# Kernel tuning notes

Hardware: AMD Instinct MI355X
Metric: run time of the kernel (lower is better)

## Reference

```python
import jax, jax.numpy as jnp
import numpy as np
import math

D_MODEL = 2048
NUM_HEADS = 32
NUM_KV_HEADS = 8
D_K = D_MODEL // NUM_HEADS  # 64
GROUPS = NUM_HEADS // NUM_KV_HEADS  # 4
WINDOW = 512
ROPE_BASE = 10000.0


def setup_inputs() -> dict:
    key = jax.random.key(0)
    ks = jax.random.split(key, 5)
    B, T = 2, 2048
    x = jax.random.normal(ks[0], (B, T, D_MODEL), dtype=jnp.float32)
    s = 0.02  # typical init scale to keep logits sane
    Wq = jax.random.normal(ks[1], (D_MODEL, D_MODEL), dtype=jnp.float32) * s
    Wk = jax.random.normal(ks[2], (NUM_KV_HEADS * D_K, D_MODEL), dtype=jnp.float32) * s
    Wv = jax.random.normal(ks[3], (NUM_KV_HEADS * D_K, D_MODEL), dtype=jnp.float32) * s
    Wo = jax.random.normal(ks[4], (D_MODEL, D_MODEL), dtype=jnp.float32) * s
    return {"x": x, "Wq": Wq, "Wk": Wk, "Wv": Wv, "Wo": Wo}


def _rotate_half(t):
    half = t.shape[-1] // 2
    return jnp.concatenate([-t[..., half:], t[..., :half]], axis=-1)


def _rope_cos_sin(T, dtype):
    inv_freq = 1.0 / (ROPE_BASE ** (jnp.arange(0, D_K, 2, dtype=jnp.float32) / D_K))
    pos = jnp.arange(T, dtype=jnp.float32)
    freqs = pos[:, None] * inv_freq[None, :]            # [T, D_K/2]
    emb = jnp.concatenate([freqs, freqs], axis=-1)       # [T, D_K]
    return jnp.cos(emb).astype(dtype)[None, None], jnp.sin(emb).astype(dtype)[None, None]


def reference(x, Wq, Wk, Wv, Wo):
    B, T, D = x.shape
    # Projections (nn.Linear: x @ W.T)
    Q = (x @ Wq.T).reshape(B, T, NUM_HEADS, D_K).transpose(0, 2, 1, 3)     # [B,H,T,dk]
    K = (x @ Wk.T).reshape(B, T, NUM_KV_HEADS, D_K).transpose(0, 2, 1, 3)  # [B,KV,T,dk]
    V = (x @ Wv.T).reshape(B, T, NUM_KV_HEADS, D_K).transpose(0, 2, 1, 3)
    # RoPE
    cos, sin = _rope_cos_sin(T, x.dtype)
    Q = Q * cos + _rotate_half(Q) * sin
    K = K * cos + _rotate_half(K) * sin
    # GQA: fold group dim into Q instead of repeat_interleave on K/V (same math)
    Qg = Q.reshape(B, NUM_KV_HEADS, GROUPS, T, D_K)
    scale = math.sqrt(D_K)
    scores = jnp.einsum('bhgqd,bhkd->bhgqk', Qg, K) / scale  # [B,KV,G,T,T]
    # sliding-window causal mask: valid iff 0 <= q_pos - k_pos < WINDOW
    pos = jnp.arange(T)
    dist = pos[:, None] - pos[None, :]
    win_mask = (dist < 0) | (dist >= WINDOW)
    scores = jnp.where(win_mask[None, None, None], -jnp.inf, scores)
    attn = jax.nn.softmax(scores, axis=-1)
    out = jnp.einsum('bhgqk,bhkd->bhgqd', attn, V)
    out = out.reshape(B, NUM_HEADS, T, D_K).transpose(0, 2, 1, 3).reshape(B, T, D)
    return out @ Wo.T
```

## Files before the change

### kernel.cpp

```cpp
#include <hip/hip_runtime.h>
#include <hip/hip_bf16.h>
#include <cstdint>
#include <cstddef>

typedef __attribute__((ext_vector_type(4))) float f32x4;
typedef __attribute__((ext_vector_type(8))) short bf16x8;
typedef __attribute__((ext_vector_type(4))) int i32x4;
typedef void __attribute__((address_space(1)))* as1_void_p;
typedef void __attribute__((address_space(3)))* as3_void_p;

#define T_SEQ 2048
#define D_MODEL 2048
#define NUM_HEADS 32
#define NUM_KV 8
#define GROUPS 4
#define DK 64
#define WINDOW 512
#define BATCH 2

#define NEG_BIG (-30000.0f)

__device__ __forceinline__ unsigned short f2b(float f) {
    unsigned int u = __builtin_bit_cast(unsigned int, f);
    u = (u + 0x7FFFu + ((u >> 16) & 1u)) >> 16;
    return (unsigned short)u;
}

__device__ __forceinline__ unsigned int cvtpk_bf16(float lo, float hi) {
    unsigned int r;
    asm("v_cvt_pk_bf16_f32 %0, %1, %2" : "=v"(r) : "v"(lo), "v"(hi));
    return r;
}

__device__ __forceinline__ void load_lds16(const void* g, void* l) {
    __builtin_amdgcn_global_load_lds((as1_void_p)(uintptr_t)g,
                                     (as3_void_p)(unsigned int)(uintptr_t)l,
                                     16, 0, 0);
}

#define CAST_N0 8388608
#define CAST_N1 12582912
#define CAST_N2 13631488
#define CAST_N3 14680064
#define CAST_N4 18874368
__global__ void cast_all_kernel(const float* __restrict__ x, const float* __restrict__ wq,
                                const float* __restrict__ wk, const float* __restrict__ wv,
                                const float* __restrict__ wo, unsigned short* __restrict__ dst) {
    int i = (blockIdx.x * blockDim.x + threadIdx.x) * 4;
    const int stride = gridDim.x * blockDim.x * 4;
    for (; i < CAST_N4; i += stride) {
        const float* src;
        int off;
        if (i < CAST_N0)      { src = x;  off = i; }
        else if (i < CAST_N1) { src = wq; off = i - CAST_N0; }
        else if (i < CAST_N2) { src = wk; off = i - CAST_N1; }
        else if (i < CAST_N3) { src = wv; off = i - CAST_N2; }
        else                  { src = wo; off = i - CAST_N3; }
        const float4 v = *(const float4*)(src + off);
        ushort4 o;
        o.x = f2b(v.x); o.y = f2b(v.y); o.z = f2b(v.z); o.w = f2b(v.w);
        *(ushort4*)(dst + i) = o;
    }
}

__global__ void rope_table_kernel(float* __restrict__ ct, float* __restrict__ st) {
    int i = blockIdx.x * blockDim.x + threadIdx.x;
    int t = i >> 5, j = i & 31;
    const float kln = 0.28782313662425556f;
    float inv = __expf(-(float)j * kln);
    if (j == 0) inv = 1.0f;
    float ang = (float)t * inv;
    float s, c;
    sincosf(ang, &s, &c);
    ct[i] = c; st[i] = s;
}


__global__ __launch_bounds__(512, 4) void gemm_qkv_rope(
    const unsigned short* __restrict__ A, const unsigned short* __restrict__ Bw,
    const float* __restrict__ ct, const float* __restrict__ st,
    unsigned short* __restrict__ Qb, unsigned short* __restrict__ Kb,
    unsigned short* __restrict__ Vt) {
    __shared__ __align__(16) unsigned short lds[32768];
    const int bid = blockIdx.x;
    const int xcd = bid & 7;
    const int l = bid >> 3;
    const int stl = l >> 4;
    const int w = l & 15;
    const int tmD = xcd * 4 + (w >> 2);
    const int tnD = stl * 4 + (w & 3);

    const int tid = threadIdx.x;
    const int lane = tid & 63;
    const int wid = tid >> 6;
    const int wr = wid >> 1, wc = wid & 1;
    const int lrow = lane & 15;
    const int g = lane >> 4;
    const int tile_m = tmD, tile_n = tnD;
    const int arow = tile_m * 128;

    const int srow = tid >> 2, sslot = tid & 3;
    const int scol0 = (sslot ^ ((srow >> 1) & 3)) << 3;

    f32x4 acc[2][4] = {};

#define QSTAGE(BUF, KCOL)                                                      \
    {                                                                          \
        load_lds16(A + (size_t)(arow + srow) * 2048 + (KCOL) + scol0,          \
                   (char*)&lds[(BUF) * 8192] + tid * 16);                      \
        load_lds16(Bw + (size_t)(tnD * 128 + srow) * 2048 + (KCOL) + scol0,    \
                   (char*)&lds[(BUF) * 8192 + 4096] + tid * 16);               \
    }

    QSTAGE(0, 0) QSTAGE(1, 32) QSTAGE(2, 64)
    asm volatile("s_waitcnt vmcnt(4)" ::: "memory");
    __builtin_amdgcn_sched_barrier(0);
    __builtin_amdgcn_s_barrier();

    for (int t = 0; t < 64; ++t) {
        const int cb = (t & 3) * 8192;
        const int sb = (t + 3) & 3;
        bf16x8 af[2], bfr[4];
#pragma unroll
        for (int m = 0; m < 2; ++m) {
            const int R = wr * 32 + m * 16 + lrow;
            af[m] = *(const bf16x8*)&lds[cb + R * 32 + ((g ^ ((R >> 1) & 3)) << 3)];
        }
#pragma unroll
        for (int n = 0; n < 4; ++n) {
            const int R = wc * 64 + n * 16 + lrow;
            bfr[n] = *(const bf16x8*)&lds[cb + 4096 + R * 32 + ((g ^ ((R >> 1) & 3)) << 3)];
        }
        if (t + 3 < 64) QSTAGE(sb, (t + 3) * 32)
        __builtin_amdgcn_s_barrier();
        asm volatile("s_waitcnt lgkmcnt(0)" ::: "memory");
        __builtin_amdgcn_sched_barrier(0);
        __builtin_amdgcn_s_setprio(1);
#pragma unroll
        for (int m = 0; m < 2; ++m)
#pragma unroll
            for (int n = 0; n < 4; ++n)
                acc[m][n] = __builtin_amdgcn_mfma_f32_16x16x32_bf16(af[m], bfr[n], acc[m][n], 0, 0, 0);
        __builtin_amdgcn_s_setprio(0);
        if (t < 63) { asm volatile("s_waitcnt vmcnt(4)" ::: "memory"); }
        else        { asm volatile("s_waitcnt vmcnt(0)" ::: "memory"); }
        __builtin_amdgcn_sched_barrier(0);
        __builtin_amdgcn_s_barrier();
    }
#undef QSTAGE

    const int hcol = tile_n * 2 + wc;
#pragma unroll
    for (int m = 0; m < 2; ++m) {
        const int row0 = tile_m * 128 + wr * 32 + m * 16 + g * 4;
        const int bb = row0 >> 11;
        const int t0 = row0 & 2047;
        if (hcol < 40) {
            const bool isQ = (hcol < 32);
            const float sc = isQ ? 0.125f : 1.0f;
            unsigned short* base = isQ
                ? (Qb + ((size_t)(bb * NUM_HEADS + hcol) * T_SEQ) * 64)
                : (Kb + ((size_t)(bb * NUM_KV + (hcol - 32)) * T_SEQ) * 64);
#pragma unroll
            for (int r = 0; r < 4; ++r) {
                const int t = t0 + r;
                unsigned short* dst = base + (size_t)t * 64;
#pragma unroll
                for (int n = 0; n < 2; ++n) {
                    const int j = n * 16 + lrow;
                    const float c = ct[t * 32 + j], s = st[t * 32 + j];
                    const float v0 = acc[m][n][r], v1 = acc[m][n + 2][r];
                    dst[j]      = f2b((v0 * c - v1 * s) * sc);
                    dst[j + 32] = f2b((v1 * c + v0 * s) * sc);
                }
            }
        } else {
            const int vh = hcol - 40;
            const int chunk = t0 >> 5, tk = t0 & 31;
            unsigned short* cbase = Vt + ((size_t)(bb * NUM_KV + vh) * 64 + chunk) * 2048 + tk;
#pragma unroll
            for (int n = 0; n < 4; ++n) {
                const int d = n * 16 + lrow;
                unsigned int u0 = cvtpk_bf16(acc[m][n][0], acc[m][n][1]);
                unsigned int u1 = cvtpk_bf16(acc[m][n][2], acc[m][n][3]);
                uint2 val; val.x = u0; val.y = u1;
                *(uint2*)(cbase + d * 32) = val;
            }
        }
    }
}

__global__ __launch_bounds__(512, 2) void gemm_bf16_nt(
    const unsigned short* __restrict__ A, const unsigned short* __restrict__ B,
    float* __restrict__ C) {
    __shared__ __align__(16) unsigned short lds[49152];
    const int bid = blockIdx.x;
    const int xcd = bid & 7;
    const int l = bid >> 3;
    const int stl = l >> 4;
    const int w = l & 15;
    const int tmD = xcd * 4 + (w >> 2);
    const int tnD = stl * 4 + (w & 3);

    const int tid = threadIdx.x;
    const int lane = tid & 63;
    const int wid = tid >> 6;
    const int wr = wid >> 2, wc = wid & 3;
    const int lrow = lane & 15;
    const int g = lane >> 4;
    const int tile_m = tmD, tile_n = tnD;
    const int arow = tile_m * 128, brow = tile_n * 256;

    const int srow = tid >> 2, sslot = tid & 3;
    const int scol = (sslot ^ ((srow >> 1) & 3)) << 3;

    f32x4 acc[4][4] = {};

#define OSTAGE(BUF, KCOL)                                                      \
    {                                                                          \
        load_lds16(A + (size_t)(arow + srow) * 2048 + (KCOL) + scol,           \
                   (char*)&lds[(BUF) * 12288] + tid * 16);                     \
        _Pragma("unroll") for (int u = 0; u < 2; ++u) {                        \
            const int gi = u * 512 + tid;                                      \
            const int br_ = gi >> 2, bs_ = gi & 3;                             \
            const int bc_ = (bs_ ^ ((br_ >> 1) & 3)) << 3;                     \
            load_lds16(B + (size_t)(brow + br_) * 2048 + (KCOL) + bc_,         \
                       (char*)&lds[(BUF) * 12288 + 4096] + gi * 16);           \
        }                                                                      \
    }

    OSTAGE(0, 0) OSTAGE(1, 32) OSTAGE(2, 64)
    asm volatile("s_waitcnt vmcnt(6)" ::: "memory");
    __builtin_amdgcn_sched_barrier(0);
    __builtin_amdgcn_s_barrier();

    for (int t = 0; t < 64; ++t) {
        const int cb = (t & 3) * 12288;
        const int sb = (t + 3) & 3;
        bf16x8 af[4], bfr[4];
#pragma unroll
        for (int m = 0; m < 4; ++m) {
            const int R = wr * 64 + m * 16 + lrow;
            af[m] = *(const bf16x8*)&lds[cb + R * 32 + ((g ^ ((R >> 1) & 3)) << 3)];
        }
#pragma unroll
        for (int n = 0; n < 4; ++n) {
            const int R = wc * 64 + n * 16 + lrow;
            bfr[n] = *(const bf16x8*)&lds[cb + 4096 + R * 32 + ((g ^ ((R >> 1) & 3)) << 3)];
        }
        if (t + 3 < 64) OSTAGE(sb, (t + 3) * 32)
        __builtin_amdgcn_s_barrier();
        asm volatile("s_waitcnt lgkmcnt(0)" ::: "memory");
        __builtin_amdgcn_sched_barrier(0);
        __builtin_amdgcn_s_setprio(1);
#pragma unroll
        for (int m = 0; m < 4; ++m)
#pragma unroll
            for (int n = 0; n < 4; ++n)
                acc[m][n] = __builtin_amdgcn_mfma_f32_16x16x32_bf16(af[m], bfr[n], acc[m][n], 0, 0, 0);
        __builtin_amdgcn_s_setprio(0);
        if (t < 63) { asm volatile("s_waitcnt vmcnt(6)" ::: "memory"); }
        else        { asm volatile("s_waitcnt vmcnt(0)" ::: "memory"); }
        __builtin_amdgcn_sched_barrier(0);
        __builtin_amdgcn_s_barrier();
    }
#undef OSTAGE

#pragma unroll
    for (int m = 0; m < 4; ++m)
#pragma unroll
        for (int n = 0; n < 4; ++n) {
            const int col = tile_n * 256 + wc * 64 + n * 16 + lrow;
#pragma unroll
            for (int r = 0; r < 4; ++r) {
                const int row = tile_m * 128 + wr * 64 + m * 16 + g * 4 + r;
                C[(size_t)row * 2048 + col] = acc[m][n][r];
            }
        }
}

__global__ __launch_bounds__(512, 4) void attn_kernel(
    const unsigned short* __restrict__ Qb, const unsigned short* __restrict__ Kb,
    const unsigned short* __restrict__ Vt, unsigned short* __restrict__ Oout) {
    __shared__ __align__(16) unsigned short lds[16384];
    const int tid = threadIdx.x;
    const int lane = tid & 63;
    const int wv = tid >> 6;
    const int g4 = wv & 3;
    const int tile = wv >> 2;
    const int bid = blockIdx.x;
    const int kvh = bid & 7;
    const int b = (bid >> 3) & 1;
    const int band = 63 - (bid >> 4);
    const int q0A = band * 32;
    const int q0w = q0A + tile * 16;
    const int h = kvh * 4 + g4;

    const int lq = lane & 15;
    const int g = lane >> 4;
    const int kq8 = g * 8;
    const int q = q0w + lq;

    const unsigned short* Qrow = Qb + ((size_t)((b * NUM_HEADS + h) * T_SEQ) + q) * 64;
    const bf16x8 qf0 = *(const bf16x8*)(Qrow + kq8);
    const bf16x8 qf1 = *(const bf16x8*)(Qrow + 32 + kq8);

    f32x4 acc[4] = {};
    float lrun = 0.0f;

    int kc_lo = q0A - (WINDOW - 1);
    if (kc_lo < 0) kc_lo = 0;
    kc_lo &= ~31;
    const int N = ((q0A - kc_lo) >> 5) + 1;

    const unsigned short* Kg = Kb + (size_t)(b * NUM_KV + kvh) * T_SEQ * 64
                                  + (size_t)kc_lo * 64;
    const unsigned short* Vg = Vt + (size_t)(b * NUM_KV + kvh) * 64 * T_SEQ
                                  + (size_t)(kc_lo >> 5) * 2048;

    const int perm = (lq >> 2) * 8 + (lq & 3);
#define SWZK(r) (((r & 3) | ((r >> 3) << 2)) & 7)
    const int koff0 = perm * 64 + ((g ^ SWZK(perm)) << 3);
    const int koff1 = perm * 64 + (((4 + g) ^ SWZK(perm)) << 3);
    const int perm4 = perm + 4;
    const int koff2 = perm4 * 64 + ((g ^ SWZK(perm4)) << 3);
    const int koff3 = perm4 * 64 + (((4 + g) ^ SWZK(perm4)) << 3);
    int voff[4];
#pragma unroll
    for (int nd = 0; nd < 4; ++nd)
        voff[nd] = 2048 + (nd * 16 + lq) * 32 + ((g ^ ((lq >> 1) & 3)) << 3);

#define STAGE(T, BUF)                                                          \
    {                                                                          \
        if (tid < 256) {                                                       \
            const int row_ = tid >> 3, ps = tid & 7;                           \
            const int ls = ps ^ SWZK(row_);                                    \
            load_lds16(Kg + (size_t)(T) * 2048 + row_ * 64 + ls * 8,           \
                       (char*)lds + (BUF) * 8192 + tid * 16);                  \
        } else {                                                               \
            const int gi = tid - 256;                                          \
            const int row_ = gi >> 2, ps = gi & 3;                             \
            const int ls = ps ^ ((row_ >> 1) & 3);                             \
            load_lds16(Vg + (size_t)(T) * 2048 + row_ * 32 + ls * 8,           \
                       (char*)lds + (BUF) * 8192 + 4096 + gi * 16);            \
        }                                                                      \
    }

    STAGE(0, 0)
    if (N > 1) STAGE(1, 1)
    if (N > 2) STAGE(2, 2)
    if (N > 2)      { asm volatile("s_waitcnt vmcnt(2)" ::: "memory"); }
    else if (N > 1) { asm volatile("s_waitcnt vmcnt(1)" ::: "memory"); }
    else            { asm volatile("s_waitcnt vmcnt(0)" ::: "memory"); }
    __builtin_amdgcn_sched_barrier(0);
    __builtin_amdgcn_s_barrier();

    for (int t = 0; t < N; ++t) {
        const int kb = (t & 3) * 4096;
        bf16x8 kf[4], vf[4];
        kf[0] = *(const bf16x8*)&lds[kb + koff0];
        kf[1] = *(const bf16x8*)&lds[kb + koff1];
        kf[2] = *(const bf16x8*)&lds[kb + koff2];
        kf[3] = *(const bf16x8*)&lds[kb + koff3];
#pragma unroll
        for (int nd = 0; nd < 4; ++nd) vf[nd] = *(const bf16x8*)&lds[kb + voff[nd]];
        if (t + 3 < N) STAGE(t + 3, (t + 3) & 3)
        asm volatile("s_waitcnt lgkmcnt(0)" ::: "memory");
        __builtin_amdgcn_sched_barrier(0);

        const int kc = kc_lo + t * 32;
        f32x4 st2[2] = {};
        st2[0] = __builtin_amdgcn_mfma_f32_16x16x32_bf16(kf[0], qf0, st2[0], 0, 0, 0);
        st2[0] = __builtin_amdgcn_mfma_f32_16x16x32_bf16(kf[1], qf1, st2[0], 0, 0, 0);
        st2[1] = __builtin_amdgcn_mfma_f32_16x16x32_bf16(kf[2], qf0, st2[1], 0, 0, 0);
        st2[1] = __builtin_amdgcn_mfma_f32_16x16x32_bf16(kf[3], qf1, st2[1], 0, 0, 0);

        float s8[8];
#pragma unroll
        for (int tt = 0; tt < 2; ++tt)
#pragma unroll
            for (int r = 0; r < 4; ++r) s8[tt * 4 + r] = st2[tt][r];

        if (kc < q0w - 496 || kc > q0w - 31) {
#pragma unroll
            for (int i = 0; i < 8; ++i) {
                const int key = kc + g * 8 + ((i >> 2) << 2) + (i & 3);
                const int dist = q - key;
                if (dist < 0 || dist >= WINDOW) s8[i] = NEG_BIG;
            }
        }

        float p8[8];
        float ps = 0.0f;
#pragma unroll
        for (int i = 0; i < 8; ++i) {
            p8[i] = __expf(s8[i]);
            ps += p8[i];
        }
        lrun += ps;

        i32x4 pwi;
        pwi[0] = (int)cvtpk_bf16(p8[0], p8[1]);
        pwi[1] = (int)cvtpk_bf16(p8[2], p8[3]);
        pwi[2] = (int)cvtpk_bf16(p8[4], p8[5]);
        pwi[3] = (int)cvtpk_bf16(p8[6], p8[7]);
        const bf16x8 pw = __builtin_bit_cast(bf16x8, pwi);

#pragma unroll
        for (int nd = 0; nd < 4; ++nd)
            acc[nd] = __builtin_amdgcn_mfma_f32_16x16x32_bf16(vf[nd], pw, acc[nd], 0, 0, 0);

        if (t + 1 < N) {
            if (t + 3 < N)      { asm volatile("s_waitcnt vmcnt(2)" ::: "memory"); }
            else if (t + 2 < N) { asm volatile("s_waitcnt vmcnt(1)" ::: "memory"); }
            else                { asm volatile("s_waitcnt vmcnt(0)" ::: "memory"); }
            __builtin_amdgcn_sched_barrier(0);
            __builtin_amdgcn_s_barrier();
        }
    }
#undef STAGE
#undef SWZK

    lrun += __shfl_xor(lrun, 16);
    lrun += __shfl_xor(lrun, 32);

    const float inv = 1.0f / lrun;
#pragma unroll
    for (int nd = 0; nd < 4; ++nd) {
        unsigned int u0 = cvtpk_bf16(acc[nd][0] * inv, acc[nd][1] * inv);
        unsigned int u1 = cvtpk_bf16(acc[nd][2] * inv, acc[nd][3] * inv);
        unsigned short* dst = Oout + ((size_t)(b * T_SEQ + q)) * D_MODEL + h * 64 + nd * 16 + g * 4;
        uint2 val; val.x = u0; val.y = u1;
        *(uint2*)dst = val;
    }
}

extern "C" void kernel_launch(void* const* d_in, const int* in_sizes, int n_in,
                              void* d_out, int out_size, void* d_ws, size_t ws_size,
                              hipStream_t stream) {
    const float* x = (const float*)d_in[0];
    const float* Wq = (const float*)d_in[1];
    const float* Wk = (const float*)d_in[2];
    const float* Wv = (const float*)d_in[3];
    const float* Wo = (const float*)d_in[4];
    float* out = (float*)d_out;

    char* ws = (char*)d_ws;
    size_t off = 0;
    auto alloc = [&](size_t bytes) -> char* {
        char* p = ws + off;
        off += (bytes + 255) & ~(size_t)255;
        return p;
    };
    unsigned short* xb   = (unsigned short*)alloc(8388608ull * 2);
    unsigned short* wcat = (unsigned short*)alloc(6291456ull * 2);
    unsigned short* wob  = (unsigned short*)alloc(4194304ull * 2);
    unsigned short* qb   = (unsigned short*)alloc(8388608ull * 2);
    unsigned short* kb   = (unsigned short*)alloc(2097152ull * 2);
    unsigned short* vt   = (unsigned short*)alloc(2097152ull * 2);
    unsigned short* attn = (unsigned short*)alloc(8388608ull * 2);
    float* ct            = (float*)alloc(65536ull * 4);
    float* st            = (float*)alloc(65536ull * 4);

    cast_all_kernel<<<2048, 256, 0, stream>>>(x, Wq, Wk, Wv, Wo, xb);
    rope_table_kernel<<<256, 256, 0, stream>>>(ct, st);

    gemm_qkv_rope<<<768, 512, 0, stream>>>(xb, wcat, ct, st, qb, kb, vt);

    attn_kernel<<<1024, 512, 0, stream>>>(qb, kb, vt, attn);

    gemm_bf16_nt<<<256, 512, 0, stream>>>(attn, wob, out);
}
```

Measured before the change: 154.5 us.

## Enlarge QKV GEMM tiles to 256x256 per block with more MFMAs per wave

The fused QKV+RoPE GEMM moves from 128x128 to 256x256 tiles per block. Each wave now computes 128x64 instead of 32x64, LDS doubles to 128KB, and the grid drops from 768 to 192 blocks. The aim is more data reuse per LDS load and less global traffic. In exchange, 192 blocks is fewer than the 256 CUs, so some CUs sit idle, and register pressure rises; the mid-loop barrier was also removed.

```diff
diff --git a/kernel.cpp b/kernel.cpp
--- a/kernel.cpp
+++ b/kernel.cpp
@@ -75,84 +75,84 @@
     ct[i] = c; st[i] = s;
 }
 
-
-__global__ __launch_bounds__(512, 4) void gemm_qkv_rope(
+__global__ __launch_bounds__(512, 2) void gemm_qkv_rope(
     const unsigned short* __restrict__ A, const unsigned short* __restrict__ Bw,
     const float* __restrict__ ct, const float* __restrict__ st,
     unsigned short* __restrict__ Qb, unsigned short* __restrict__ Kb,
     unsigned short* __restrict__ Vt) {
-    __shared__ __align__(16) unsigned short lds[32768];
+    __shared__ __align__(16) unsigned short lds[65536];
     const int bid = blockIdx.x;
     const int xcd = bid & 7;
     const int l = bid >> 3;
-    const int stl = l >> 4;
-    const int w = l & 15;
-    const int tmD = xcd * 4 + (w >> 2);
-    const int tnD = stl * 4 + (w & 3);
+    const int stl = l >> 2;
+    const int w = l & 3;
+    const int tile_m = xcd * 2 + (w >> 1);
+    const int tile_n = stl * 2 + (w & 1);
 
     const int tid = threadIdx.x;
     const int lane = tid & 63;
     const int wid = tid >> 6;
-    const int wr = wid >> 1, wc = wid & 1;
+    const int wr = wid >> 2, wc = wid & 3;
     const int lrow = lane & 15;
     const int g = lane >> 4;
-    const int tile_m = tmD, tile_n = tnD;
-    const int arow = tile_m * 128;
-
-    const int srow = tid >> 2, sslot = tid & 3;
-    const int scol0 = (sslot ^ ((srow >> 1) & 3)) << 3;
-
-    f32x4 acc[2][4] = {};
-
-#define QSTAGE(BUF, KCOL)                                                      \
-    {                                                                          \
-        load_lds16(A + (size_t)(arow + srow) * 2048 + (KCOL) + scol0,          \
-                   (char*)&lds[(BUF) * 8192] + tid * 16);                      \
-        load_lds16(Bw + (size_t)(tnD * 128 + srow) * 2048 + (KCOL) + scol0,    \
-                   (char*)&lds[(BUF) * 8192 + 4096] + tid * 16);               \
-    }
-
-    QSTAGE(0, 0) QSTAGE(1, 32) QSTAGE(2, 64)
-    asm volatile("s_waitcnt vmcnt(4)" ::: "memory");
+    const int arow = tile_m * 256, brow = tile_n * 256;
+
+    f32x4 acc[8][4] = {};
+
+#define QSTAGE(SRC, ROWBASE, KCOL, USHOFF)                                     \
+    { _Pragma("unroll") for (int u = 0; u < 2; ++u) {                          \
+        const int gi = u * 512 + tid;                                          \
+        const int row_ = gi >> 2, sl_ = gi & 3;                                \
+        const int sc_ = (sl_ ^ ((row_ >> 1) & 3)) << 3;                        \
+        load_lds16(SRC + (size_t)((ROWBASE) + row_) * 2048 + (KCOL) + sc_,     \
+                   (char*)&lds[USHOFF] + gi * 16); } }
+
+    QSTAGE(A, arow, 0,  0)     QSTAGE(Bw, brow, 0,  8192)
+    QSTAGE(A, arow, 32, 16384) QSTAGE(Bw, brow, 32, 24576)
+    QSTAGE(A, arow, 64, 32768) QSTAGE(Bw, brow, 64, 40960)
+    asm volatile("s_waitcnt vmcnt(8)" ::: "memory");
     __builtin_amdgcn_sched_barrier(0);
     __builtin_amdgcn_s_barrier();
 
     for (int t = 0; t < 64; ++t) {
-        const int cb = (t & 3) * 8192;
-        const int sb = (t + 3) & 3;
-        bf16x8 af[2], bfr[4];
-#pragma unroll
-        for (int m = 0; m < 2; ++m) {
-            const int R = wr * 32 + m * 16 + lrow;
+        const int cb = (t & 3) * 16384;
+        const int sb = ((t + 3) & 3) * 16384;
+        bf16x8 af[8], bfr[4];
+#pragma unroll
+        for (int m = 0; m < 8; ++m) {
+            const int R = wr * 128 + m * 16 + lrow;
             af[m] = *(const bf16x8*)&lds[cb + R * 32 + ((g ^ ((R >> 1) & 3)) << 3)];
         }
 #pragma unroll
         for (int n = 0; n < 4; ++n) {
             const int R = wc * 64 + n * 16 + lrow;
-            bfr[n] = *(const bf16x8*)&lds[cb + 4096 + R * 32 + ((g ^ ((R >> 1) & 3)) << 3)];
-        }
-        if (t + 3 < 64) QSTAGE(sb, (t + 3) * 32)
-        __builtin_amdgcn_s_barrier();
+            bfr[n] = *(const bf16x8*)&lds[cb + 8192 + R * 32 + ((g ^ ((R >> 1) & 3)) << 3)];
+        }
+        if (t + 3 < 64) {
+            QSTAGE(A, arow, (t + 3) * 32, sb)
+            QSTAGE(Bw, brow, (t + 3) * 32, sb + 8192)
+        }
         asm volatile("s_waitcnt lgkmcnt(0)" ::: "memory");
         __builtin_amdgcn_sched_barrier(0);
         __builtin_amdgcn_s_setprio(1);
 #pragma unroll
-        for (int m = 0; m < 2; ++m)
+        for (int m = 0; m < 8; ++m)
 #pragma unroll
             for (int n = 0; n < 4; ++n)
                 acc[m][n] = __builtin_amdgcn_mfma_f32_16x16x32_bf16(af[m], bfr[n], acc[m][n], 0, 0, 0);
         __builtin_amdgcn_s_setprio(0);
-        if (t < 63) { asm volatile("s_waitcnt vmcnt(4)" ::: "memory"); }
-        else        { asm volatile("s_waitcnt vmcnt(0)" ::: "memory"); }
+        if (t < 61)      { asm volatile("s_waitcnt vmcnt(8)" ::: "memory"); }
+        else if (t == 61){ asm volatile("s_waitcnt vmcnt(4)" ::: "memory"); }
+        else             { asm volatile("s_waitcnt vmcnt(0)" ::: "memory"); }
         __builtin_amdgcn_sched_barrier(0);
         __builtin_amdgcn_s_barrier();
     }
 #undef QSTAGE
 
-    const int hcol = tile_n * 2 + wc;
-#pragma unroll
-    for (int m = 0; m < 2; ++m) {
-        const int row0 = tile_m * 128 + wr * 32 + m * 16 + g * 4;
+    const int hcol = tile_n * 4 + wc;
+#pragma unroll
+    for (int m = 0; m < 8; ++m) {
+        const int row0 = tile_m * 256 + wr * 128 + m * 16 + g * 4;
         const int bb = row0 >> 11;
         const int t0 = row0 & 2047;
         if (hcol < 40) {
@@ -465,7 +465,7 @@
     cast_all_kernel<<<2048, 256, 0, stream>>>(x, Wq, Wk, Wv, Wo, xb);
     rope_table_kernel<<<256, 256, 0, stream>>>(ct, st);
 
-    gemm_qkv_rope<<<768, 512, 0, stream>>>(xb, wcat, ct, st, qb, kb, vt);
+    gemm_qkv_rope<<<192, 512, 0, stream>>>(xb, wcat, ct, st, qb, kb, vt);
 
     attn_kernel<<<1024, 512, 0, stream>>>(qb, kb, vt, attn);
 
```

Measured after the change: 150.0 us. 2.9% less time.
